# Performance work log

Measured on AMD Instinct MI355X. Metric: run time of the kernel, lower is better.

Reference implementation:

```python
import jax, jax.numpy as jnp
import numpy as np

N, G, D, F, A = 50000, 128, 32, 64, 8
N_ITERS, N_BLAYERS = 3, 3
EPS = 1e-5
HIN = D + F + 2 * F * A  # 1120: input to transform_out


def setup_inputs() -> dict:
    key = jax.random.key(0)
    ks = jax.random.split(key, 10)
    p = lambda k, shape: jax.random.normal(k, shape, jnp.float32) * 0.05
    return {
        "x": jax.random.normal(ks[0], (N, 3), jnp.float32),
        "batch": jnp.sort(jax.random.randint(ks[1], (N,), 0, G)),
        # input_network: Linear(3,D) + LayerNorm(D) + Tanh
        "Wi": p(ks[2], (3, D)), "bi": jnp.zeros((D,), jnp.float32),
        "lni_w": jnp.ones((D,), jnp.float32), "lni_b": jnp.zeros((D,), jnp.float32),
        # 3 BipartiteLayers (weights shared across graph iterations, stacked over layer idx)
        "W_in": p(ks[3], (N_BLAYERS, D, F)), "b_in": jnp.zeros((N_BLAYERS, F), jnp.float32),
        "W_sc": p(ks[4], (N_BLAYERS, F, A)), "b_sc": jnp.zeros((N_BLAYERS, A), jnp.float32),
        "W_out": p(ks[5], (N_BLAYERS, HIN, D)), "b_out": jnp.zeros((N_BLAYERS, D), jnp.float32),
        # PyG graph-mode LayerNorm after each BipartiteLayer
        "gln_w": jnp.ones((N_BLAYERS, D), jnp.float32), "gln_b": jnp.zeros((N_BLAYERS, D), jnp.float32),
        "Wp": p(ks[6], (3, D, D)), "bp": jnp.zeros((3, D), jnp.float32),
        "lnp_w": jnp.ones((3, D), jnp.float32), "lnp_b": jnp.zeros((3, D), jnp.float32),
        "Wpo": p(ks[7], (D, 1)), "bpo": jnp.zeros((1,), jnp.float32),
    }


def _ln(x, w, b):  # nn.LayerNorm over last dim
    m = x.mean(-1, keepdims=True)
    v = ((x - m) ** 2).mean(-1, keepdims=True)
    return (x - m) / jnp.sqrt(v + EPS) * w + b


def _graph_ln(x, w, b):  # PyG gnn.norm.LayerNorm, mode='graph', batch=None
    xc = x - x.mean()
    std = jnp.sqrt((xc * xc).mean())
    return xc / (std + EPS) * w + b


def _bipartite(x, batch, counts, Win, bin_, Wsc, bsc, Wout, bout):
    xp = x @ Win + bin_                                  # (N,F)
    attn = jnp.exp(-jnp.abs(xp @ Wsc + bsc))             # (N,A) 'potential' activation
    w = attn[:, :, None] * xp[:, None, :]                # (N,A,F) == einsum('nf,na->naf')
    sums = jax.ops.segment_sum(w, batch, num_segments=G)  # (G,A,F)
    cnt = counts[:, None, None]
    mean_p = sums / jnp.maximum(cnt, 1.0)
    max_p = jax.ops.segment_max(w, batch, num_segments=G)
    max_p = jnp.where(cnt > 0, max_p, 0.0)               # torch_scatter zero-fill for empty
    agg = jnp.concatenate([mean_p, max_p], axis=-1).reshape(G, 2 * F * A)  # (G,A,2F)->(G,2FA)
    H = jnp.concatenate([x, xp, agg[batch]], axis=-1)    # (N, HIN)
    return jnp.tanh(H @ Wout + bout)                     # Tanh hidden activation


def reference(x, batch, Wi, bi, lni_w, lni_b, W_in, b_in, W_sc, b_sc, W_out, b_out,
              gln_w, gln_b, Wp, bp, lnp_w, lnp_b, Wpo, bpo):
    counts = jax.ops.segment_sum(jnp.ones((x.shape[0],), x.dtype), batch, num_segments=G)
    h = jnp.tanh(_ln(x @ Wi + bi, lni_w, lni_b))
    for _ in range(N_ITERS):
        for j in range(N_BLAYERS):
            h = _bipartite(h, batch, counts, W_in[j], b_in[j], W_sc[j], b_sc[j], W_out[j], b_out[j])
            h = _graph_ln(h, gln_w[j], gln_b[j])
    s = jax.ops.segment_sum(h, batch, num_segments=G) / jnp.maximum(counts, 1.0)[:, None]  # scatter_mean
    for j in range(3):
        s = jnp.tanh(_ln(s @ Wp[j] + bp[j], lnp_w[j], lnp_b[j]))
    return (s @ Wpo + bpo).squeeze(-1)  # (G,)
```

## Files before the change

### kernel.cpp

```cpp
#include <hip/hip_runtime.h>
#include <math.h>

#define NPTS 50000
#define NG   128
#define DD   32
#define FF   64
#define AA   8
#define HINC 1120
#define EPSV 1e-5f
#define CH   64

__device__ __forceinline__ float tanh_fast(float x) {
    float e = __expf(-2.f * fabsf(x));
    float r = __fdividef(1.f - e, 1.f + e);
    return copysignf(r, x);
}

__global__ __launch_bounds__(256) void k_setup(const int* __restrict__ batch,
                                               const float* __restrict__ W_in,
                                               const float* __restrict__ b_in,
                                               const float* __restrict__ W_out,
                                               const float* __restrict__ b_out,
                                               int* __restrict__ offs,
                                               float* __restrict__ stats,
                                               float* __restrict__ Weff,
                                               float* __restrict__ beff) {
    int t = threadIdx.x, bid = blockIdx.x;
    if (bid == 0) {
        if (t <= NG) {
            int lo = 0, hi = NPTS;
            while (lo < hi) { int mid = (lo+hi)>>1; if (batch[mid] < t) lo = mid+1; else hi = mid; }
            offs[t] = lo;
        }
        if (t < 32) stats[t] = 0.f;
    } else {
        int j = bid - 1;
        const float* W0 = W_out + (size_t)j*HINC*DD;
        const float* W1 = W0 + DD*DD;
        const float* Wi = W_in + (size_t)j*DD*FF;
        for (int e = t; e < DD*DD; e += 256) {
            int i = e >> 5, d = e & 31;
            float s = W0[e];
            for (int f = 0; f < FF; f++) s += Wi[i*FF+f] * W1[f*DD+d];
            Weff[j*DD*DD + e] = s;
        }
        if (t < DD) {
            float s = b_out[j*DD + t];
            for (int f = 0; f < FF; f++) s += b_in[j*FF+f] * W1[f*DD+t];
            beff[j*DD + t] = s;
        }
    }
}

__global__ __launch_bounds__(512) void k_L(const float* __restrict__ x,
                                           const float* __restrict__ Wi,
                                           const float* __restrict__ bi,
                                           const float* __restrict__ lniw,
                                           const float* __restrict__ lnib,
                                           const float* __restrict__ inb,
                                           const float* __restrict__ stats,
                                           const float* __restrict__ gw,
                                           const float* __restrict__ gb,
                                           const float* __restrict__ Win,
                                           const float* __restrict__ bin,
                                           const float* __restrict__ Wsc,
                                           const float* __restrict__ bsc,
                                           const int* __restrict__ offs,
                                           float* __restrict__ hout,
                                           const float* __restrict__ Wagg,
                                           const float* __restrict__ beff,
                                           const float* __restrict__ Weff,
                                           float* __restrict__ tbuf,
                                           float* __restrict__ statsO,
                                           int isL0) {
    int g = blockIdx.x;
    int gs = offs[g], cnt = offs[g+1] - gs;
    const int t = threadIdx.x;
    if (cnt <= 0) return;

    __shared__ float hs[CH][36];
    __shared__ float sxp[CH][68];
    __shared__ float sattn[CH][9];
    __shared__ float sWin[DD*FF];
    __shared__ float sScT[AA*FF];
    __shared__ float sW[DD][36];
    __shared__ float agg[2*FF*AA];
    __shared__ float red[16][DD];
    __shared__ float aggWs[DD];
    __shared__ float rs1[8], rs2[8];

    ((float4*)sWin)[t] = ((const float4*)Win)[t];
    { int a = t >> 6, f = t & 63; sScT[t] = Wsc[f*AA + a]; }
    for (int k = t; k < DD*DD; k += 512) sW[k >> 5][k & 31] = Weff[k];

    float gm = 0.f, ginv = 1.f;
    if (stats) {
        const float invM = 1.f/((float)NPTS*DD);
        gm = stats[0]*invM;
        float var = stats[1]*invM - gm*gm;
        ginv = 1.f/(sqrtf(fmaxf(var, 0.f)) + EPSV);
    }

    const int pt = t >> 3, q = t & 7;
    const int fo = q * 8;
    const int ca = t >> 6, cf = t & 63;
    const float bscv = bsc[q];
    const float4 bi0 = *(const float4*)&bin[fo];
    const float4 bi1 = *(const float4*)&bin[fo+4];
    float csum = 0.f, cmax = -INFINITY;

    for (int base = gs; base < gs + cnt; base += CH) {
        int np = min(CH, gs + cnt - base);
        __syncthreads();
        {
            int pp = t >> 3, d4 = (t & 7)*4;
            if (pp < np) {
                int n = base + pp;
                if (isL0) {
                    float x0 = x[n*3], x1 = x[n*3+1], x2 = x[n*3+2];
                    float tv0 = x0*Wi[d4+0] + x1*Wi[DD+d4+0] + x2*Wi[2*DD+d4+0] + bi[d4+0];
                    float tv1 = x0*Wi[d4+1] + x1*Wi[DD+d4+1] + x2*Wi[2*DD+d4+1] + bi[d4+1];
                    float tv2 = x0*Wi[d4+2] + x1*Wi[DD+d4+2] + x2*Wi[2*DD+d4+2] + bi[d4+2];
                    float tv3 = x0*Wi[d4+3] + x1*Wi[DD+d4+3] + x2*Wi[2*DD+d4+3] + bi[d4+3];
                    float sm = (tv0+tv1) + (tv2+tv3);
                    sm += __shfl_xor(sm, 1); sm += __shfl_xor(sm, 2); sm += __shfl_xor(sm, 4);
                    float mm = sm * (1.f/DD);
                    float c0 = tv0-mm, c1 = tv1-mm, c2 = tv2-mm, c3 = tv3-mm;
                    float qq = (c0*c0 + c1*c1) + (c2*c2 + c3*c3);
                    qq += __shfl_xor(qq, 1); qq += __shfl_xor(qq, 2); qq += __shfl_xor(qq, 4);
                    float inv = 1.f/sqrtf(qq*(1.f/DD) + EPSV);
                    float o0 = tanh_fast(c0*inv*lniw[d4+0] + lnib[d4+0]);
                    float o1 = tanh_fast(c1*inv*lniw[d4+1] + lnib[d4+1]);
                    float o2 = tanh_fast(c2*inv*lniw[d4+2] + lnib[d4+2]);
                    float o3 = tanh_fast(c3*inv*lniw[d4+3] + lnib[d4+3]);
                    hs[pp][d4+0] = o0; hs[pp][d4+1] = o1; hs[pp][d4+2] = o2; hs[pp][d4+3] = o3;
                    *(float4*)&hout[(size_t)n*DD + d4] = make_float4(o0,o1,o2,o3);
                } else {
                    float4 v = *(const float4*)&inb[(size_t)n*DD + d4];
                    float4 w4 = make_float4(1,1,1,1), b4 = make_float4(0,0,0,0);
                    if (gw) { w4 = *(const float4*)&gw[d4]; b4 = *(const float4*)&gb[d4]; }
                    hs[pp][d4+0] = (v.x-gm)*ginv*w4.x + b4.x;
                    hs[pp][d4+1] = (v.y-gm)*ginv*w4.y + b4.y;
                    hs[pp][d4+2] = (v.z-gm)*ginv*w4.z + b4.z;
                    hs[pp][d4+3] = (v.w-gm)*ginv*w4.w + b4.w;
                }
            }
        }
        __syncthreads();
        if (pt < np) {
            float xr[8] = {bi0.x,bi0.y,bi0.z,bi0.w,bi1.x,bi1.y,bi1.z,bi1.w};
            #pragma unroll
            for (int k = 0; k < DD; k++) {
                float hv = hs[pt][k];
                float4 wa = *(const float4*)&sWin[k*FF + fo];
                float4 wb = *(const float4*)&sWin[k*FF + fo + 4];
                xr[0] += hv*wa.x; xr[1] += hv*wa.y; xr[2] += hv*wa.z; xr[3] += hv*wa.w;
                xr[4] += hv*wb.x; xr[5] += hv*wb.y; xr[6] += hv*wb.z; xr[7] += hv*wb.w;
            }
            float pa[8];
            #pragma unroll
            for (int a = 0; a < 8; a++) {
                float4 wa = *(const float4*)&sScT[a*FF + fo];
                float4 wb = *(const float4*)&sScT[a*FF + fo + 4];
                pa[a] = xr[0]*wa.x + xr[1]*wa.y + xr[2]*wa.z + xr[3]*wa.w
                      + xr[4]*wb.x + xr[5]*wb.y + xr[6]*wb.z + xr[7]*wb.w;
            }
            #pragma unroll
            for (int msk = 1; msk < 8; msk <<= 1) {
                #pragma unroll
                for (int a = 0; a < 8; a++) pa[a] += __shfl_xor(pa[a], msk);
            }
            sattn[pt][q] = __expf(-fabsf(pa[q] + bscv));
            *(float4*)&sxp[pt][fo]   = make_float4(xr[0],xr[1],xr[2],xr[3]);
            *(float4*)&sxp[pt][fo+4] = make_float4(xr[4],xr[5],xr[6],xr[7]);
        }
        __syncthreads();
        for (int pp = 0; pp < np; pp++) {
            float w = sattn[pp][ca] * sxp[pp][cf];
            csum += w; cmax = fmaxf(cmax, w);
        }
    }

    agg[ca*2*FF + cf]      = csum / (float)cnt;
    agg[ca*2*FF + FF + cf] = cmax;
    __syncthreads();
    {
        int d = t & 31, grp = t >> 5;
        float acc = 0.f;
        #pragma unroll
        for (int k2 = 0; k2 < 64; k2++) {
            int k = grp*64 + k2;
            acc += agg[k] * Wagg[k*DD + d];
        }
        red[grp][d] = acc;
    }
    __syncthreads();
    if (t < DD) {
        float r = 0.f;
        #pragma unroll
        for (int qq = 0; qq < 16; qq++) r += red[qq][t];
        aggWs[t] = r + beff[t];
    }

    float s1 = 0.f, s2a = 0.f;
    for (int base = gs; base < gs + cnt; base += CH) {
        int np = min(CH, gs + cnt - base);
        __syncthreads();
        {
            int pp = t >> 3, d4 = (t & 7)*4;
            if (pp < np) {
                int n = base + pp;
                if (isL0) {
                    float x0 = x[n*3], x1 = x[n*3+1], x2 = x[n*3+2];
                    float tv0 = x0*Wi[d4+0] + x1*Wi[DD+d4+0] + x2*Wi[2*DD+d4+0] + bi[d4+0];
                    float tv1 = x0*Wi[d4+1] + x1*Wi[DD+d4+1] + x2*Wi[2*DD+d4+1] + bi[d4+1];
                    float tv2 = x0*Wi[d4+2] + x1*Wi[DD+d4+2] + x2*Wi[2*DD+d4+2] + bi[d4+2];
                    float tv3 = x0*Wi[d4+3] + x1*Wi[DD+d4+3] + x2*Wi[2*DD+d4+3] + bi[d4+3];
                    float sm = (tv0+tv1) + (tv2+tv3);
                    sm += __shfl_xor(sm, 1); sm += __shfl_xor(sm, 2); sm += __shfl_xor(sm, 4);
                    float mm = sm * (1.f/DD);
                    float c0 = tv0-mm, c1 = tv1-mm, c2 = tv2-mm, c3 = tv3-mm;
                    float qq = (c0*c0 + c1*c1) + (c2*c2 + c3*c3);
                    qq += __shfl_xor(qq, 1); qq += __shfl_xor(qq, 2); qq += __shfl_xor(qq, 4);
                    float inv = 1.f/sqrtf(qq*(1.f/DD) + EPSV);
                    hs[pp][d4+0] = tanh_fast(c0*inv*lniw[d4+0] + lnib[d4+0]);
                    hs[pp][d4+1] = tanh_fast(c1*inv*lniw[d4+1] + lnib[d4+1]);
                    hs[pp][d4+2] = tanh_fast(c2*inv*lniw[d4+2] + lnib[d4+2]);
                    hs[pp][d4+3] = tanh_fast(c3*inv*lniw[d4+3] + lnib[d4+3]);
                } else {
                    float4 v = *(const float4*)&inb[(size_t)n*DD + d4];
                    float4 w4 = make_float4(1,1,1,1), b4 = make_float4(0,0,0,0);
                    if (gw) { w4 = *(const float4*)&gw[d4]; b4 = *(const float4*)&gb[d4]; }
                    hs[pp][d4+0] = (v.x-gm)*ginv*w4.x + b4.x;
                    hs[pp][d4+1] = (v.y-gm)*ginv*w4.y + b4.y;
                    hs[pp][d4+2] = (v.z-gm)*ginv*w4.z + b4.z;
                    hs[pp][d4+3] = (v.w-gm)*ginv*w4.w + b4.w;
                }
            }
        }
        __syncthreads();
        {
            int pp = t >> 3, d4 = (t & 7)*4;
            if (pp < np) {
                int n = base + pp;
                float4 a0 = *(const float4*)&aggWs[d4];
                float acc0 = a0.x, acc1 = a0.y, acc2 = a0.z, acc3 = a0.w;
                #pragma unroll
                for (int k = 0; k < DD; k++) {
                    float hv = hs[pp][k];
                    float4 w = *(const float4*)&sW[k][d4];
                    acc0 += hv*w.x; acc1 += hv*w.y; acc2 += hv*w.z; acc3 += hv*w.w;
                }
                float4 o;
                o.x = tanh_fast(acc0); o.y = tanh_fast(acc1);
                o.z = tanh_fast(acc2); o.w = tanh_fast(acc3);
                *(float4*)&tbuf[(size_t)n*DD + d4] = o;
                s1  += (o.x + o.y) + (o.z + o.w);
                s2a += (o.x*o.x + o.y*o.y) + (o.z*o.z + o.w*o.w);
            }
        }
    }
    #pragma unroll
    for (int o = 32; o > 0; o >>= 1) { s1 += __shfl_down(s1, o); s2a += __shfl_down(s2a, o); }
    int wid = t >> 6;
    if ((t & 63) == 0) { rs1[wid] = s1; rs2[wid] = s2a; }
    __syncthreads();
    if (t == 0) {
        float a1 = 0.f, a2 = 0.f;
        #pragma unroll
        for (int qq = 0; qq < 8; qq++) { a1 += rs1[qq]; a2 += rs2[qq]; }
        atomicAdd(&statsO[0], a1);
        atomicAdd(&statsO[1], a2);
    }
}

__global__ __launch_bounds__(256) void k_read(const float* __restrict__ tbuf,
                                              const float* __restrict__ stats,
                                              const float* __restrict__ gw,
                                              const float* __restrict__ gb,
                                              const int* __restrict__ offs,
                                              const float* __restrict__ Wp,
                                              const float* __restrict__ bp,
                                              const float* __restrict__ lnw,
                                              const float* __restrict__ lnb,
                                              const float* __restrict__ Wpo,
                                              const float* __restrict__ bpo,
                                              float* __restrict__ out) {
    int g = blockIdx.x;
    int t = threadIdx.x;
    int d = t & 31, pl = t >> 5;
    int s0 = offs[g], e0 = offs[g+1];
    float acc = 0.f;
    for (int n = s0 + pl; n < e0; n += 8) acc += tbuf[(size_t)n*DD + d];
    __shared__ float red[8][DD];
    red[pl][d] = acc;
    __syncthreads();
    __shared__ float sv[DD];
    if (t < DD) {
        float r = 0.f;
        #pragma unroll
        for (int qq = 0; qq < 8; qq++) r += red[qq][t];
        const float invM = 1.f/((float)NPTS*DD);
        float m = stats[0]*invM;
        float var = stats[1]*invM - m*m;
        float inv = 1.f/(sqrtf(fmaxf(var, 0.f)) + EPSV);
        float cnt = (float)(e0 - s0);
        float mean = r / fmaxf(cnt, 1.f);
        sv[t] = (e0 > s0) ? (mean - m)*inv*gw[t] + gb[t] : 0.f;
    }
    __syncthreads();
    for (int j = 0; j < 3; j++) {
        float yv = 0.f;
        if (t < DD) {
            float y = bp[j*DD + t];
            #pragma unroll
            for (int i = 0; i < DD; i++) y += sv[i] * Wp[j*DD*DD + i*DD + t];
            float sum = y;
            #pragma unroll
            for (int o = 1; o < 32; o <<= 1) sum += __shfl_xor(sum, o);
            float m = sum * (1.f/DD);
            float c = y - m;
            float sq = c*c;
            #pragma unroll
            for (int o = 1; o < 32; o <<= 1) sq += __shfl_xor(sq, o);
            float var = sq * (1.f/DD);
            yv = tanh_fast(c / sqrtf(var + EPSV) * lnw[j*DD+t] + lnb[j*DD+t]);
        }
        __syncthreads();
        if (t < DD) sv[t] = yv;
        __syncthreads();
    }
    if (t < DD) {
        float p = sv[t] * Wpo[t];
        #pragma unroll
        for (int o = 1; o < 32; o <<= 1) p += __shfl_xor(p, o);
        if (t == 0) out[g] = p + bpo[0];
    }
}

extern "C" void kernel_launch(void* const* d_in, const int* in_sizes, int n_in,
                              void* d_out, int out_size, void* d_ws, size_t ws_size,
                              hipStream_t stream) {
    const float* x     = (const float*)d_in[0];
    const int*   batch = (const int*)  d_in[1];
    const float* Wi    = (const float*)d_in[2];
    const float* bi    = (const float*)d_in[3];
    const float* lni_w = (const float*)d_in[4];
    const float* lni_b = (const float*)d_in[5];
    const float* W_in  = (const float*)d_in[6];
    const float* b_in  = (const float*)d_in[7];
    const float* W_sc  = (const float*)d_in[8];
    const float* b_sc  = (const float*)d_in[9];
    const float* W_out = (const float*)d_in[10];
    const float* b_out = (const float*)d_in[11];
    const float* gln_w = (const float*)d_in[12];
    const float* gln_b = (const float*)d_in[13];
    const float* Wp    = (const float*)d_in[14];
    const float* bp    = (const float*)d_in[15];
    const float* lnp_w = (const float*)d_in[16];
    const float* lnp_b = (const float*)d_in[17];
    const float* Wpo   = (const float*)d_in[18];
    const float* bpo   = (const float*)d_in[19];
    float* out = (float*)d_out;

    float* ws    = (float*)d_ws;
    float* h     = ws;
    float* tbuf  = h + (size_t)NPTS*DD;
    float* stats = tbuf + (size_t)NPTS*DD;
    float* Weff  = stats + 32;
    float* beff  = Weff + 3*DD*DD;
    int*   offs  = (int*)(beff + 3*DD);

    k_setup<<<4, 256, 0, stream>>>(batch, W_in, b_in, W_out, b_out, offs, stats, Weff, beff);

    for (int L = 0; L < 9; ++L) {
        int j = L % 3;
        int pj = (L + 2) % 3;
        const float* inb = L ? tbuf : h;
        const float* st  = L ? stats + 2*(L-1) : nullptr;
        const float* pgw = L ? gln_w + pj*DD : nullptr;
        const float* pgb = L ? gln_b + pj*DD : nullptr;
        k_L<<<NG, 512, 0, stream>>>(
            x, Wi, bi, lni_w, lni_b,
            inb, st, pgw, pgb,
            W_in + (size_t)j*DD*FF, b_in + j*FF,
            W_sc + (size_t)j*FF*AA, b_sc + j*AA,
            offs, h,
            W_out + (size_t)j*HINC*DD + (size_t)96*DD, beff + j*DD,
            Weff + (size_t)j*DD*DD, tbuf, stats + 2*L, (L == 0) ? 1 : 0);
    }
    k_read<<<NG, 256, 0, stream>>>(tbuf, stats + 16, gln_w + 2*DD, gln_b + 2*DD,
                                   offs, Wp, bp, lnp_w, lnp_b, Wpo, bpo, out);
}
```

Before: 371.7 us.

## Fold graph LayerNorm into weights and stream node rows through registers

For layers after the first, the per-layer graph LayerNorm scale and shift are folded into the W_in and Weff weights held in shared memory, with the shift terms moved into adjusted biases. Raw node features can then be loaded straight into registers with a one-chunk-ahead prefetch, instead of being normalised and staged through shared memory. The second pass drops its shared-memory staging and barriers in the same way, and layer 0 recomputes the input network rather than writing a separate h buffer. In exchange, each block does a small per-layer weight rescale at the start, register pressure rises from the prefetch buffers, and rounding changes slightly because normalisation is applied through the weights.

Result: faster. 352.5 us (-5.2%).

```diff
diff --git a/kernel.cpp b/kernel.cpp
--- a/kernel.cpp
+++ b/kernel.cpp
@@ -66,7 +66,6 @@
                                            const float* __restrict__ Wsc,
                                            const float* __restrict__ bsc,
                                            const int* __restrict__ offs,
-                                           float* __restrict__ hout,
                                            const float* __restrict__ Wagg,
                                            const float* __restrict__ beff,
                                            const float* __restrict__ Weff,
@@ -87,6 +86,8 @@
     __shared__ float agg[2*FF*AA];
     __shared__ float red[16][DD];
     __shared__ float aggWs[DD];
+    __shared__ float sbin[FF];
+    __shared__ float shW[DD];
     __shared__ float rs1[8], rs2[8];
 
     ((float4*)sWin)[t] = ((const float4*)Win)[t];
@@ -94,123 +95,58 @@
     for (int k = t; k < DD*DD; k += 512) sW[k >> 5][k & 31] = Weff[k];
 
     float gm = 0.f, ginv = 1.f;
-    if (stats) {
+    if (!isL0) {
         const float invM = 1.f/((float)NPTS*DD);
         gm = stats[0]*invM;
         float var = stats[1]*invM - gm*gm;
         ginv = 1.f/(sqrtf(fmaxf(var, 0.f)) + EPSV);
     }
+    __syncthreads();
+    if (!isL0) {
+        if (t < FF) {
+            float b = bin[t];
+            for (int k = 0; k < DD; k++) {
+                float sk = ginv * gw[k];
+                float sh = gb[k] - gm * sk;
+                b += sh * sWin[k*FF + t];
+            }
+            sbin[t] = b;
+        } else if (t < FF + DD) {
+            int d = t - FF;
+            float r = 0.f;
+            for (int k = 0; k < DD; k++) {
+                float sk = ginv * gw[k];
+                float sh = gb[k] - gm * sk;
+                r += sh * sW[k][d];
+            }
+            shW[d] = r;
+        }
+        __syncthreads();
+        for (int e = t; e < DD*FF; e += 512) sWin[e] *= ginv * gw[e >> 6];
+        for (int e = t; e < DD*DD; e += 512) sW[e >> 5][e & 31] *= ginv * gw[e >> 5];
+        __syncthreads();
+    } else {
+        if (t < FF) sbin[t] = bin[t];
+        else if (t < FF + DD) shW[t - FF] = 0.f;
+        __syncthreads();
+    }
 
     const int pt = t >> 3, q = t & 7;
     const int fo = q * 8;
     const int ca = t >> 6, cf = t & 63;
     const float bscv = bsc[q];
-    const float4 bi0 = *(const float4*)&bin[fo];
-    const float4 bi1 = *(const float4*)&bin[fo+4];
+    const float4 bi0 = *(const float4*)&sbin[fo];
+    const float4 bi1 = *(const float4*)&sbin[fo+4];
     float csum = 0.f, cmax = -INFINITY;
 
-    for (int base = gs; base < gs + cnt; base += CH) {
-        int np = min(CH, gs + cnt - base);
-        __syncthreads();
-        {
-            int pp = t >> 3, d4 = (t & 7)*4;
-            if (pp < np) {
-                int n = base + pp;
-                if (isL0) {
-                    float x0 = x[n*3], x1 = x[n*3+1], x2 = x[n*3+2];
-                    float tv0 = x0*Wi[d4+0] + x1*Wi[DD+d4+0] + x2*Wi[2*DD+d4+0] + bi[d4+0];
-                    float tv1 = x0*Wi[d4+1] + x1*Wi[DD+d4+1] + x2*Wi[2*DD+d4+1] + bi[d4+1];
-                    float tv2 = x0*Wi[d4+2] + x1*Wi[DD+d4+2] + x2*Wi[2*DD+d4+2] + bi[d4+2];
-                    float tv3 = x0*Wi[d4+3] + x1*Wi[DD+d4+3] + x2*Wi[2*DD+d4+3] + bi[d4+3];
-                    float sm = (tv0+tv1) + (tv2+tv3);
-                    sm += __shfl_xor(sm, 1); sm += __shfl_xor(sm, 2); sm += __shfl_xor(sm, 4);
-                    float mm = sm * (1.f/DD);
-                    float c0 = tv0-mm, c1 = tv1-mm, c2 = tv2-mm, c3 = tv3-mm;
-                    float qq = (c0*c0 + c1*c1) + (c2*c2 + c3*c3);
-                    qq += __shfl_xor(qq, 1); qq += __shfl_xor(qq, 2); qq += __shfl_xor(qq, 4);
-                    float inv = 1.f/sqrtf(qq*(1.f/DD) + EPSV);
-                    float o0 = tanh_fast(c0*inv*lniw[d4+0] + lnib[d4+0]);
-                    float o1 = tanh_fast(c1*inv*lniw[d4+1] + lnib[d4+1]);
-                    float o2 = tanh_fast(c2*inv*lniw[d4+2] + lnib[d4+2]);
-                    float o3 = tanh_fast(c3*inv*lniw[d4+3] + lnib[d4+3]);
-                    hs[pp][d4+0] = o0; hs[pp][d4+1] = o1; hs[pp][d4+2] = o2; hs[pp][d4+3] = o3;
-                    *(float4*)&hout[(size_t)n*DD + d4] = make_float4(o0,o1,o2,o3);
-                } else {
-                    float4 v = *(const float4*)&inb[(size_t)n*DD + d4];
-                    float4 w4 = make_float4(1,1,1,1), b4 = make_float4(0,0,0,0);
-                    if (gw) { w4 = *(const float4*)&gw[d4]; b4 = *(const float4*)&gb[d4]; }
-                    hs[pp][d4+0] = (v.x-gm)*ginv*w4.x + b4.x;
-                    hs[pp][d4+1] = (v.y-gm)*ginv*w4.y + b4.y;
-                    hs[pp][d4+2] = (v.z-gm)*ginv*w4.z + b4.z;
-                    hs[pp][d4+3] = (v.w-gm)*ginv*w4.w + b4.w;
-                }
-            }
-        }
-        __syncthreads();
-        if (pt < np) {
-            float xr[8] = {bi0.x,bi0.y,bi0.z,bi0.w,bi1.x,bi1.y,bi1.z,bi1.w};
-            #pragma unroll
-            for (int k = 0; k < DD; k++) {
-                float hv = hs[pt][k];
-                float4 wa = *(const float4*)&sWin[k*FF + fo];
-                float4 wb = *(const float4*)&sWin[k*FF + fo + 4];
-                xr[0] += hv*wa.x; xr[1] += hv*wa.y; xr[2] += hv*wa.z; xr[3] += hv*wa.w;
-                xr[4] += hv*wb.x; xr[5] += hv*wb.y; xr[6] += hv*wb.z; xr[7] += hv*wb.w;
-            }
-            float pa[8];
-            #pragma unroll
-            for (int a = 0; a < 8; a++) {
-                float4 wa = *(const float4*)&sScT[a*FF + fo];
-                float4 wb = *(const float4*)&sScT[a*FF + fo + 4];
-                pa[a] = xr[0]*wa.x + xr[1]*wa.y + xr[2]*wa.z + xr[3]*wa.w
-                      + xr[4]*wb.x + xr[5]*wb.y + xr[6]*wb.z + xr[7]*wb.w;
-            }
-            #pragma unroll
-            for (int msk = 1; msk < 8; msk <<= 1) {
-                #pragma unroll
-                for (int a = 0; a < 8; a++) pa[a] += __shfl_xor(pa[a], msk);
-            }
-            sattn[pt][q] = __expf(-fabsf(pa[q] + bscv));
-            *(float4*)&sxp[pt][fo]   = make_float4(xr[0],xr[1],xr[2],xr[3]);
-            *(float4*)&sxp[pt][fo+4] = make_float4(xr[4],xr[5],xr[6],xr[7]);
-        }
-        __syncthreads();
-        for (int pp = 0; pp < np; pp++) {
-            float w = sattn[pp][ca] * sxp[pp][cf];
-            csum += w; cmax = fmaxf(cmax, w);
-        }
-    }
-
-    agg[ca*2*FF + cf]      = csum / (float)cnt;
-    agg[ca*2*FF + FF + cf] = cmax;
-    __syncthreads();
-    {
-        int d = t & 31, grp = t >> 5;
-        float acc = 0.f;
-        #pragma unroll
-        for (int k2 = 0; k2 < 64; k2++) {
-            int k = grp*64 + k2;
-            acc += agg[k] * Wagg[k*DD + d];
-        }
-        red[grp][d] = acc;
-    }
-    __syncthreads();
-    if (t < DD) {
-        float r = 0.f;
-        #pragma unroll
-        for (int qq = 0; qq < 16; qq++) r += red[qq][t];
-        aggWs[t] = r + beff[t];
-    }
-
-    float s1 = 0.f, s2a = 0.f;
-    for (int base = gs; base < gs + cnt; base += CH) {
-        int np = min(CH, gs + cnt - base);
-        __syncthreads();
-        {
-            int pp = t >> 3, d4 = (t & 7)*4;
-            if (pp < np) {
-                int n = base + pp;
-                if (isL0) {
+    if (isL0) {
+        for (int base = gs; base < gs + cnt; base += CH) {
+            int np = min(CH, gs + cnt - base);
+            __syncthreads();
+            {
+                int pp = t >> 3, d4 = (t & 7)*4;
+                if (pp < np) {
+                    int n = base + pp;
                     float x0 = x[n*3], x1 = x[n*3+1], x2 = x[n*3+2];
                     float tv0 = x0*Wi[d4+0] + x1*Wi[DD+d4+0] + x2*Wi[2*DD+d4+0] + bi[d4+0];
                     float tv1 = x0*Wi[d4+1] + x1*Wi[DD+d4+1] + x2*Wi[2*DD+d4+1] + bi[d4+1];
@@ -227,29 +163,210 @@
                     hs[pp][d4+1] = tanh_fast(c1*inv*lniw[d4+1] + lnib[d4+1]);
                     hs[pp][d4+2] = tanh_fast(c2*inv*lniw[d4+2] + lnib[d4+2]);
                     hs[pp][d4+3] = tanh_fast(c3*inv*lniw[d4+3] + lnib[d4+3]);
-                } else {
-                    float4 v = *(const float4*)&inb[(size_t)n*DD + d4];
-                    float4 w4 = make_float4(1,1,1,1), b4 = make_float4(0,0,0,0);
-                    if (gw) { w4 = *(const float4*)&gw[d4]; b4 = *(const float4*)&gb[d4]; }
-                    hs[pp][d4+0] = (v.x-gm)*ginv*w4.x + b4.x;
-                    hs[pp][d4+1] = (v.y-gm)*ginv*w4.y + b4.y;
-                    hs[pp][d4+2] = (v.z-gm)*ginv*w4.z + b4.z;
-                    hs[pp][d4+3] = (v.w-gm)*ginv*w4.w + b4.w;
-                }
-            }
-        }
-        __syncthreads();
+                }
+            }
+            __syncthreads();
+            if (pt < np) {
+                float xr[8] = {bi0.x,bi0.y,bi0.z,bi0.w,bi1.x,bi1.y,bi1.z,bi1.w};
+                #pragma unroll
+                for (int k = 0; k < DD; k++) {
+                    float hv = hs[pt][k];
+                    float4 wa = *(const float4*)&sWin[k*FF + fo];
+                    float4 wb = *(const float4*)&sWin[k*FF + fo + 4];
+                    xr[0] += hv*wa.x; xr[1] += hv*wa.y; xr[2] += hv*wa.z; xr[3] += hv*wa.w;
+                    xr[4] += hv*wb.x; xr[5] += hv*wb.y; xr[6] += hv*wb.z; xr[7] += hv*wb.w;
+                }
+                float pa[8];
+                #pragma unroll
+                for (int a = 0; a < 8; a++) {
+                    float4 wa = *(const float4*)&sScT[a*FF + fo];
+                    float4 wb = *(const float4*)&sScT[a*FF + fo + 4];
+                    pa[a] = xr[0]*wa.x + xr[1]*wa.y + xr[2]*wa.z + xr[3]*wa.w
+                          + xr[4]*wb.x + xr[5]*wb.y + xr[6]*wb.z + xr[7]*wb.w;
+                }
+                #pragma unroll
+                for (int msk = 1; msk < 8; msk <<= 1) {
+                    #pragma unroll
+                    for (int a = 0; a < 8; a++) pa[a] += __shfl_xor(pa[a], msk);
+                }
+                sattn[pt][q] = __expf(-fabsf(pa[q] + bscv));
+                *(float4*)&sxp[pt][fo]   = make_float4(xr[0],xr[1],xr[2],xr[3]);
+                *(float4*)&sxp[pt][fo+4] = make_float4(xr[4],xr[5],xr[6],xr[7]);
+            }
+            __syncthreads();
+            for (int pp = 0; pp < np; pp++) {
+                float w = sattn[pp][ca] * sxp[pp][cf];
+                csum += w; cmax = fmaxf(cmax, w);
+            }
+        }
+    } else {
+        float4 cur[8], nxt[8];
         {
-            int pp = t >> 3, d4 = (t & 7)*4;
-            if (pp < np) {
-                int n = base + pp;
-                float4 a0 = *(const float4*)&aggWs[d4];
+            int n0 = gs + min(pt, cnt-1);
+            const float4* r4 = (const float4*)(inb + (size_t)n0*DD);
+            #pragma unroll
+            for (int j = 0; j < 8; j++) cur[j] = r4[j];
+        }
+        for (int base = gs; base < gs + cnt; base += CH) {
+            int np = min(CH, gs + cnt - base);
+            {
+                int nb = base + CH;
+                int nclamp = (nb < gs + cnt) ? min(nb + pt, gs + cnt - 1) : gs;
+                const float4* r4 = (const float4*)(inb + (size_t)nclamp*DD);
+                #pragma unroll
+                for (int j = 0; j < 8; j++) nxt[j] = r4[j];
+            }
+            __syncthreads();
+            if (pt < np) {
+                float xr[8] = {bi0.x,bi0.y,bi0.z,bi0.w,bi1.x,bi1.y,bi1.z,bi1.w};
+                #pragma unroll
+                for (int k4 = 0; k4 < 8; k4++) {
+                    float hv0 = cur[k4].x, hv1 = cur[k4].y, hv2 = cur[k4].z, hv3 = cur[k4].w;
+                    int kb = k4*4;
+                    float4 wa, wb;
+                    wa = *(const float4*)&sWin[(kb+0)*FF + fo]; wb = *(const float4*)&sWin[(kb+0)*FF + fo + 4];
+                    xr[0]+=hv0*wa.x; xr[1]+=hv0*wa.y; xr[2]+=hv0*wa.z; xr[3]+=hv0*wa.w;
+                    xr[4]+=hv0*wb.x; xr[5]+=hv0*wb.y; xr[6]+=hv0*wb.z; xr[7]+=hv0*wb.w;
+                    wa = *(const float4*)&sWin[(kb+1)*FF + fo]; wb = *(const float4*)&sWin[(kb+1)*FF + fo + 4];
+                    xr[0]+=hv1*wa.x; xr[1]+=hv1*wa.y; xr[2]+=hv1*wa.z; xr[3]+=hv1*wa.w;
+                    xr[4]+=hv1*wb.x; xr[5]+=hv1*wb.y; xr[6]+=hv1*wb.z; xr[7]+=hv1*wb.w;
+                    wa = *(const float4*)&sWin[(kb+2)*FF + fo]; wb = *(const float4*)&sWin[(kb+2)*FF + fo + 4];
+                    xr[0]+=hv2*wa.x; xr[1]+=hv2*wa.y; xr[2]+=hv2*wa.z; xr[3]+=hv2*wa.w;
+                    xr[4]+=hv2*wb.x; xr[5]+=hv2*wb.y; xr[6]+=hv2*wb.z; xr[7]+=hv2*wb.w;
+                    wa = *(const float4*)&sWin[(kb+3)*FF + fo]; wb = *(const float4*)&sWin[(kb+3)*FF + fo + 4];
+                    xr[0]+=hv3*wa.x; xr[1]+=hv3*wa.y; xr[2]+=hv3*wa.z; xr[3]+=hv3*wa.w;
+                    xr[4]+=hv3*wb.x; xr[5]+=hv3*wb.y; xr[6]+=hv3*wb.z; xr[7]+=hv3*wb.w;
+                }
+                float pa[8];
+                #pragma unroll
+                for (int a = 0; a < 8; a++) {
+                    float4 wa = *(const float4*)&sScT[a*FF + fo];
+                    float4 wb = *(const float4*)&sScT[a*FF + fo + 4];
+                    pa[a] = xr[0]*wa.x + xr[1]*wa.y + xr[2]*wa.z + xr[3]*wa.w
+                          + xr[4]*wb.x + xr[5]*wb.y + xr[6]*wb.z + xr[7]*wb.w;
+                }
+                #pragma unroll
+                for (int msk = 1; msk < 8; msk <<= 1) {
+                    #pragma unroll
+                    for (int a = 0; a < 8; a++) pa[a] += __shfl_xor(pa[a], msk);
+                }
+                sattn[pt][q] = __expf(-fabsf(pa[q] + bscv));
+                *(float4*)&sxp[pt][fo]   = make_float4(xr[0],xr[1],xr[2],xr[3]);
+                *(float4*)&sxp[pt][fo+4] = make_float4(xr[4],xr[5],xr[6],xr[7]);
+            }
+            __syncthreads();
+            for (int pp = 0; pp < np; pp++) {
+                float w = sattn[pp][ca] * sxp[pp][cf];
+                csum += w; cmax = fmaxf(cmax, w);
+            }
+            #pragma unroll
+            for (int j = 0; j < 8; j++) cur[j] = nxt[j];
+        }
+    }
+
+    agg[ca*2*FF + cf]      = csum / (float)cnt;
+    agg[ca*2*FF + FF + cf] = cmax;
+    __syncthreads();
+    {
+        int d = t & 31, grp = t >> 5;
+        float acc = 0.f;
+        #pragma unroll
+        for (int k2 = 0; k2 < 64; k2++) {
+            int k = grp*64 + k2;
+            acc += agg[k] * Wagg[k*DD + d];
+        }
+        red[grp][d] = acc;
+    }
+    __syncthreads();
+    if (t < DD) {
+        float r = 0.f;
+        #pragma unroll
+        for (int qq = 0; qq < 16; qq++) r += red[qq][t];
+        aggWs[t] = r + beff[t] + shW[t];
+    }
+    __syncthreads();
+
+    float s1 = 0.f, s2a = 0.f;
+    const int d4 = q * 4;
+    if (isL0) {
+        for (int base = gs; base < gs + cnt; base += CH) {
+            int np = min(CH, gs + cnt - base);
+            __syncthreads();
+            {
+                int pp = t >> 3;
+                if (pp < np) {
+                    int n = base + pp;
+                    float x0 = x[n*3], x1 = x[n*3+1], x2 = x[n*3+2];
+                    float tv0 = x0*Wi[d4+0] + x1*Wi[DD+d4+0] + x2*Wi[2*DD+d4+0] + bi[d4+0];
+                    float tv1 = x0*Wi[d4+1] + x1*Wi[DD+d4+1] + x2*Wi[2*DD+d4+1] + bi[d4+1];
+                    float tv2 = x0*Wi[d4+2] + x1*Wi[DD+d4+2] + x2*Wi[2*DD+d4+2] + bi[d4+2];
+                    float tv3 = x0*Wi[d4+3] + x1*Wi[DD+d4+3] + x2*Wi[2*DD+d4+3] + bi[d4+3];
+                    float sm = (tv0+tv1) + (tv2+tv3);
+                    sm += __shfl_xor(sm, 1); sm += __shfl_xor(sm, 2); sm += __shfl_xor(sm, 4);
+                    float mm = sm * (1.f/DD);
+                    float c0 = tv0-mm, c1 = tv1-mm, c2 = tv2-mm, c3 = tv3-mm;
+                    float qq = (c0*c0 + c1*c1) + (c2*c2 + c3*c3);
+                    qq += __shfl_xor(qq, 1); qq += __shfl_xor(qq, 2); qq += __shfl_xor(qq, 4);
+                    float inv = 1.f/sqrtf(qq*(1.f/DD) + EPSV);
+                    hs[pp][d4+0] = tanh_fast(c0*inv*lniw[d4+0] + lnib[d4+0]);
+                    hs[pp][d4+1] = tanh_fast(c1*inv*lniw[d4+1] + lnib[d4+1]);
+                    hs[pp][d4+2] = tanh_fast(c2*inv*lniw[d4+2] + lnib[d4+2]);
+                    hs[pp][d4+3] = tanh_fast(c3*inv*lniw[d4+3] + lnib[d4+3]);
+                }
+            }
+            __syncthreads();
+            {
+                int pp = t >> 3;
+                if (pp < np) {
+                    int n = base + pp;
+                    float4 a0 = *(const float4*)&aggWs[d4];
+                    float acc0 = a0.x, acc1 = a0.y, acc2 = a0.z, acc3 = a0.w;
+                    #pragma unroll
+                    for (int k = 0; k < DD; k++) {
+                        float hv = hs[pp][k];
+                        float4 w = *(const float4*)&sW[k][d4];
+                        acc0 += hv*w.x; acc1 += hv*w.y; acc2 += hv*w.z; acc3 += hv*w.w;
+                    }
+                    float4 o;
+                    o.x = tanh_fast(acc0); o.y = tanh_fast(acc1);
+                    o.z = tanh_fast(acc2); o.w = tanh_fast(acc3);
+                    *(float4*)&tbuf[(size_t)n*DD + d4] = o;
+                    s1  += (o.x + o.y) + (o.z + o.w);
+                    s2a += (o.x*o.x + o.y*o.y) + (o.z*o.z + o.w*o.w);
+                }
+            }
+        }
+    } else {
+        float4 rcur[8], rnxt[8];
+        if (pt < cnt) {
+            {
+                const float4* r4 = (const float4*)(inb + (size_t)(gs + pt)*DD);
+                #pragma unroll
+                for (int j = 0; j < 8; j++) rcur[j] = r4[j];
+            }
+            float4 a0 = *(const float4*)&aggWs[d4];
+            for (int n = gs + pt; n < gs + cnt; n += CH) {
+                int nn = n + CH;
+                int nclamp = (nn < gs + cnt) ? nn : n;
+                {
+                    const float4* r4 = (const float4*)(inb + (size_t)nclamp*DD);
+                    #pragma unroll
+                    for (int j = 0; j < 8; j++) rnxt[j] = r4[j];
+                }
                 float acc0 = a0.x, acc1 = a0.y, acc2 = a0.z, acc3 = a0.w;
                 #pragma unroll
-                for (int k = 0; k < DD; k++) {
-                    float hv = hs[pp][k];
-                    float4 w = *(const float4*)&sW[k][d4];
-                    acc0 += hv*w.x; acc1 += hv*w.y; acc2 += hv*w.z; acc3 += hv*w.w;
+                for (int k4 = 0; k4 < 8; k4++) {
+                    float hv0 = rcur[k4].x, hv1 = rcur[k4].y, hv2 = rcur[k4].z, hv3 = rcur[k4].w;
+                    int kb = k4*4;
+                    float4 w;
+                    w = *(const float4*)&sW[kb+0][d4];
+                    acc0 += hv0*w.x; acc1 += hv0*w.y; acc2 += hv0*w.z; acc3 += hv0*w.w;
+                    w = *(const float4*)&sW[kb+1][d4];
+                    acc0 += hv1*w.x; acc1 += hv1*w.y; acc2 += hv1*w.z; acc3 += hv1*w.w;
+                    w = *(const float4*)&sW[kb+2][d4];
+                    acc0 += hv2*w.x; acc1 += hv2*w.y; acc2 += hv2*w.z; acc3 += hv2*w.w;
+                    w = *(const float4*)&sW[kb+3][d4];
+                    acc0 += hv3*w.x; acc1 += hv3*w.y; acc2 += hv3*w.z; acc3 += hv3*w.w;
                 }
                 float4 o;
                 o.x = tanh_fast(acc0); o.y = tanh_fast(acc1);
@@ -257,12 +374,15 @@
                 *(float4*)&tbuf[(size_t)n*DD + d4] = o;
                 s1  += (o.x + o.y) + (o.z + o.w);
                 s2a += (o.x*o.x + o.y*o.y) + (o.z*o.z + o.w*o.w);
+                #pragma unroll
+                for (int j = 0; j < 8; j++) rcur[j] = rnxt[j];
             }
         }
     }
     #pragma unroll
     for (int o = 32; o > 0; o >>= 1) { s1 += __shfl_down(s1, o); s2a += __shfl_down(s2a, o); }
     int wid = t >> 6;
+    __syncthreads();
     if ((t & 63) == 0) { rs1[wid] = s1; rs2[wid] = s2a; }
     __syncthreads();
     if (t == 0) {
@@ -364,8 +484,7 @@
     float* out = (float*)d_out;
 
     float* ws    = (float*)d_ws;
-    float* h     = ws;
-    float* tbuf  = h + (size_t)NPTS*DD;
+    float* tbuf  = ws;
     float* stats = tbuf + (size_t)NPTS*DD;
     float* Weff  = stats + 32;
     float* beff  = Weff + 3*DD*DD;
@@ -376,16 +495,15 @@
     for (int L = 0; L < 9; ++L) {
         int j = L % 3;
         int pj = (L + 2) % 3;
-        const float* inb = L ? tbuf : h;
         const float* st  = L ? stats + 2*(L-1) : nullptr;
         const float* pgw = L ? gln_w + pj*DD : nullptr;
         const float* pgb = L ? gln_b + pj*DD : nullptr;
         k_L<<<NG, 512, 0, stream>>>(
             x, Wi, bi, lni_w, lni_b,
-            inb, st, pgw, pgb,
+            tbuf, st, pgw, pgb,
             W_in + (size_t)j*DD*FF, b_in + j*FF,
             W_sc + (size_t)j*FF*AA, b_sc + j*AA,
-            offs, h,
+            offs,
             W_out + (size_t)j*HINC*DD + (size_t)96*DD, beff + j*DD,
             Weff + (size_t)j*DD*DD, tbuf, stats + 2*L, (L == 0) ? 1 : 0);
     }
```
